# Optimization experiments

Measured on AMD Instinct MI355X. Metric: run time of the kernel, lower is better.

The kernel has to match this reference:

```python
import jax, jax.numpy as jnp
import numpy as np

B, NF, FD, ND, C, K, L = 32, 64, 64, 256, 8, 6, 2  # batch, num_frames(feat), fused_dim, nodes, edge channels, neighbors, layers


def setup_inputs() -> dict:
    key = jax.random.key(0)
    ks = jax.random.split(key, 6)
    s = lambda k, shape: jax.random.normal(k, shape, jnp.float32) * 0.05
    return {
        "fused": jax.random.normal(ks[0], (B, NF, FD), jnp.float32),
        "w1": s(ks[1], (NF, FD, FD)),
        "b1": jnp.zeros((NF, 1, FD), jnp.float32),
        "w2": s(ks[2], (NF, FD, ND)),
        "b2": jnp.zeros((NF, 1, ND), jnp.float32),
        "edge_qk_w": s(ks[3], (2 * C * NF, NF)),
        "ga_qk_w": s(ks[4], (L, 2 * NF, NF)),
        "ga_qk_b": jnp.zeros((L, 2 * NF), jnp.float32),
        "ga_w": jnp.ones((L, 1, C), jnp.float32),
    }


def _spec_norm(w):
    # per-node spectral normalization (torch does this in-place under no_grad)
    n = jax.lax.stop_gradient(jnp.linalg.norm(w, ord=2, axis=(1, 2), keepdims=True))
    return w / jnp.clip(n, 1e-6, None)


def _forward(fused, w1, b1, w2, b2, edge_qk_w, ga_qk_w, ga_qk_b, ga_w):
    scale = NF ** -0.5
    # --- MultiNodeMlp (per-frame node-wise MLP) ---
    h = jnp.einsum('bni,nij->bnj', fused, _spec_norm(w1)) + b1[:, 0]
    h = jax.nn.gelu(h, approximate=False)
    conv = jnp.einsum('bni,nio->bno', h, _spec_norm(w2)) + b2[:, 0]  # [B,NF,ND]
    x = conv.transpose(0, 2, 1)  # node features [B,ND,NF]

    # --- EdgeLayer: multi-channel attention + top-k clip + double normalization ---
    qk = (x @ edge_qk_w.T).reshape(B, ND, 2, C, NF)
    q = qk[:, :, 0].transpose(0, 2, 1, 3)  # [B,C,ND,NF]
    k = qk[:, :, 1].transpose(0, 2, 1, 3)
    attn = jax.nn.softmax(jnp.einsum('bcnf,bcmf->bcnm', q, k) * scale, axis=-1)
    sum_edge = jax.lax.stop_gradient(attn).sum(axis=1)            # [B,ND,ND]
    top_idx = jax.lax.top_k(sum_edge, K)[1]                       # [B,ND,K]
    onehot = jnp.clip(jax.nn.one_hot(top_idx, ND, dtype=attn.dtype).sum(axis=2), 0.0, 1.0)
    mask = jnp.maximum(onehot, jnp.eye(ND, dtype=attn.dtype))[:, None]  # [B,1,ND,ND]
    masked = mask * attn
    nr = masked / (masked.sum(-1, keepdims=True) + 1e-6)
    nc = nr / (nr.sum(-2, keepdims=True) + 1e-6)
    edge = jnp.einsum('bcnd,bcmd->bcnm', nr, nc)                  # norm_row @ norm_col^T

    # --- LipschitzGraph: residual invertible graph attention layers ---
    eye = jnp.eye(NF, dtype=x.dtype)
    for l in range(L):
        W, bqk, wch = ga_qk_w[l], ga_qk_b[l], ga_w[l]
        xs = jax.nn.sigmoid(jax.nn.elu(x))
        qkx = xs @ W.T + bqk                                       # [B,ND,2NF]
        qg, kg = qkx[..., :NF], qkx[..., NF:]
        a = jax.nn.softmax(jnp.einsum('bnf,bmf->bnm', qg, kg) * scale, axis=-1)
        ne = a[:, None] * edge                                     # [B,C,ND,ND]
        ne = ne / (ne.sum(-1, keepdims=True) + 1e-6)
        ne = jnp.einsum('bcnd,c->bnd', ne, (wch / wch.sum())[0])
        dot = W[:NF] @ W[NF:].T * scale
        lip = jax.lax.stop_gradient(jnp.linalg.norm(eye + 2.0 * dot, ord=2)) + 5.0
        x = x + (ne @ xs) / lip
    return x


def reference(fused, w1, b1, w2, b2, edge_qk_w, ga_qk_w, ga_qk_b, ga_w):
    return _forward(fused, w1, b1, w2, b2, edge_qk_w, ga_qk_w, ga_qk_b, ga_w)
```

## Files before the change

kernel.cpp:

```cpp
#include <hip/hip_runtime.h>
#include <float.h>
#include <math.h>


typedef short bf8t __attribute__((ext_vector_type(8)));
typedef float f4t __attribute__((ext_vector_type(4)));

static __device__ __forceinline__ unsigned short f2bf(float x) {
  union { float f; unsigned u; } v; v.f = x;
  unsigned r = (v.u + 0x7FFFu + ((v.u >> 16) & 1u)) >> 16;
  return (unsigned short)r;
}
static __device__ __forceinline__ float bf2f(unsigned short s) {
  union { unsigned u; float f; } v; v.u = ((unsigned)s) << 16; return v.f;
}
static __device__ __forceinline__ float bf2f_lo(unsigned u) {
  union { unsigned u; float f; } v; v.u = u << 16; return v.f;
}
static __device__ __forceinline__ float bf2f_hi(unsigned u) {
  union { unsigned u; float f; } v; v.u = u & 0xFFFF0000u; return v.f;
}
static __device__ __forceinline__ float dot3_pair(unsigned uqh, unsigned uql,
                                                  unsigned ukh, unsigned ukl) {
  float s = bf2f_lo(uqh) * (bf2f_lo(ukh) + bf2f_lo(ukl)) + bf2f_lo(uql) * bf2f_lo(ukh);
  s += bf2f_hi(uqh) * (bf2f_hi(ukh) + bf2f_hi(ukl)) + bf2f_hi(uql) * bf2f_hi(ukh);
  return s;
}
static __device__ __forceinline__ void split8(const float* __restrict__ p,
                                              bf8t* hi, bf8t* lo) {
  float4 v0 = *(const float4*)(p);
  float4 v1 = *(const float4*)(p + 4);
  float v[8] = {v0.x, v0.y, v0.z, v0.w, v1.x, v1.y, v1.z, v1.w};
#pragma unroll
  for (int j = 0; j < 8; j++) {
    unsigned short h = f2bf(v[j]);
    (*hi)[j] = (short)h;
    (*lo)[j] = (short)f2bf(v[j] - bf2f(h));
  }
}

#define SPAD 68

static __device__ __forceinline__ void mm_mfma(
    const float* __restrict__ A, const float* __restrict__ B,
    float* __restrict__ C, int t, float scale, int addI, int transposeStore) {
  int wv = t >> 6, l = t & 63;
  int m16 = l & 15, quad = l >> 4;
  bf8t ah[2], al[2];
  const float* ap = A + (size_t)(16 * wv + m16) * SPAD + quad * 8;
  split8(ap, &ah[0], &al[0]);
  split8(ap + 32, &ah[1], &al[1]);
  f4t acc[4];
#pragma unroll
  for (int ct = 0; ct < 4; ct++) {
    bf8t bh[2], bl[2];
    const float* bp = B + (size_t)(ct * 16 + m16) * SPAD + quad * 8;
    split8(bp, &bh[0], &bl[0]);
    split8(bp + 32, &bh[1], &bl[1]);
    f4t a = (f4t){0.f, 0.f, 0.f, 0.f};
    a = __builtin_amdgcn_mfma_f32_16x16x32_bf16(al[0], bh[0], a, 0, 0, 0);
    a = __builtin_amdgcn_mfma_f32_16x16x32_bf16(ah[0], bl[0], a, 0, 0, 0);
    a = __builtin_amdgcn_mfma_f32_16x16x32_bf16(ah[0], bh[0], a, 0, 0, 0);
    a = __builtin_amdgcn_mfma_f32_16x16x32_bf16(al[1], bh[1], a, 0, 0, 0);
    a = __builtin_amdgcn_mfma_f32_16x16x32_bf16(ah[1], bl[1], a, 0, 0, 0);
    a = __builtin_amdgcn_mfma_f32_16x16x32_bf16(ah[1], bh[1], a, 0, 0, 0);
    acc[ct] = a;
  }
#pragma unroll
  for (int ct = 0; ct < 4; ct++)
#pragma unroll
    for (int j = 0; j < 4; j++) {
      int i0 = 16 * wv + quad * 4 + j;
      int j0 = ct * 16 + m16;
      float v = acc[ct][j] * scale + ((addI && i0 == j0) ? 1.0f : 0.0f);
      if (transposeStore) C[(size_t)j0 * SPAD + i0] = v;
      else C[(size_t)i0 * SPAD + j0] = v;
    }
}

static __device__ __forceinline__ void mm_sq_norm(
    const float* __restrict__ A, float* __restrict__ C, int t,
    float* __restrict__ redm) {
  int wv = t >> 6, l = t & 63;
  int m16 = l & 15, quad = l >> 4;
  bf8t ah[2], al[2];
  const float* ap = A + (size_t)(16 * wv + m16) * SPAD + quad * 8;
  split8(ap, &ah[0], &al[0]);
  split8(ap + 32, &ah[1], &al[1]);
  f4t acc[4];
#pragma unroll
  for (int ct = 0; ct < 4; ct++) {
    bf8t bh[2], bl[2];
    const float* bp = A + (size_t)(ct * 16 + m16) * SPAD + quad * 8;
    split8(bp, &bh[0], &bl[0]);
    split8(bp + 32, &bh[1], &bl[1]);
    f4t a = (f4t){0.f, 0.f, 0.f, 0.f};
    a = __builtin_amdgcn_mfma_f32_16x16x32_bf16(al[0], bh[0], a, 0, 0, 0);
    a = __builtin_amdgcn_mfma_f32_16x16x32_bf16(ah[0], bl[0], a, 0, 0, 0);
    a = __builtin_amdgcn_mfma_f32_16x16x32_bf16(ah[0], bh[0], a, 0, 0, 0);
    a = __builtin_amdgcn_mfma_f32_16x16x32_bf16(al[1], bh[1], a, 0, 0, 0);
    a = __builtin_amdgcn_mfma_f32_16x16x32_bf16(ah[1], bl[1], a, 0, 0, 0);
    a = __builtin_amdgcn_mfma_f32_16x16x32_bf16(ah[1], bh[1], a, 0, 0, 0);
    acc[ct] = a;
  }
  float mx = 0.f;
#pragma unroll
  for (int ct = 0; ct < 4; ct++)
#pragma unroll
    for (int j = 0; j < 4; j++) mx = fmaxf(mx, fabsf(acc[ct][j]));
#pragma unroll
  for (int m = 1; m < 64; m <<= 1) mx = fmaxf(mx, __shfl_xor(mx, m, 64));
  if (l == 0) redm[wv] = mx;
  __syncthreads();
  float gmx = fmaxf(fmaxf(redm[0], redm[1]), fmaxf(redm[2], redm[3]));
  float sc = 1.0f / fmaxf(gmx, 1e-30f);
#pragma unroll
  for (int ct = 0; ct < 4; ct++)
#pragma unroll
    for (int j = 0; j < 4; j++)
      C[(size_t)(16 * wv + quad * 4 + j) * SPAD + ct * 16 + m16] = acc[ct][j] * sc;
}

static __device__ __forceinline__ void gram_mfma(
    const float* __restrict__ Ag, int ncols, float* __restrict__ S,
    float* __restrict__ G, int t) {
  int wv = t >> 6, l = t & 63;
  int m16 = l & 15, quad = l >> 4;
  f4t acc[4];
#pragma unroll
  for (int ct = 0; ct < 4; ct++) acc[ct] = (f4t){0.f, 0.f, 0.f, 0.f};
  for (int cc = 0; cc < ncols; cc += 64) {
    if (cc) __syncthreads();
    for (int i = t; i < 1024; i += 256) {
      int r = i >> 4, qq = i & 15;
      float4 v = *(const float4*)(Ag + (size_t)r * ncols + cc + 4 * qq);
      *(float4*)(S + (size_t)r * SPAD + 4 * qq) = v;
    }
    __syncthreads();
    bf8t ah[2], al[2];
    const float* ap = S + (size_t)(16 * wv + m16) * SPAD + quad * 8;
    split8(ap, &ah[0], &al[0]);
    split8(ap + 32, &ah[1], &al[1]);
#pragma unroll
    for (int ct = 0; ct < 4; ct++) {
      bf8t bh[2], bl[2];
      const float* bp = S + (size_t)(ct * 16 + m16) * SPAD + quad * 8;
      split8(bp, &bh[0], &bl[0]);
      split8(bp + 32, &bh[1], &bl[1]);
      f4t a = acc[ct];
      a = __builtin_amdgcn_mfma_f32_16x16x32_bf16(al[0], bh[0], a, 0, 0, 0);
      a = __builtin_amdgcn_mfma_f32_16x16x32_bf16(ah[0], bl[0], a, 0, 0, 0);
      a = __builtin_amdgcn_mfma_f32_16x16x32_bf16(ah[0], bh[0], a, 0, 0, 0);
      a = __builtin_amdgcn_mfma_f32_16x16x32_bf16(al[1], bh[1], a, 0, 0, 0);
      a = __builtin_amdgcn_mfma_f32_16x16x32_bf16(ah[1], bl[1], a, 0, 0, 0);
      a = __builtin_amdgcn_mfma_f32_16x16x32_bf16(ah[1], bh[1], a, 0, 0, 0);
      acc[ct] = a;
    }
  }
  __syncthreads();
#pragma unroll
  for (int ct = 0; ct < 4; ct++)
#pragma unroll
    for (int j = 0; j < 4; j++)
      G[(size_t)(16 * wv + quad * 4 + j) * SPAD + ct * 16 + m16] = acc[ct][j];
}

static __device__ __forceinline__ float power_rayleigh(
    const float* __restrict__ G4m, const float* __restrict__ Gm, int iters, int i) {
  float row[64];
#pragma unroll
  for (int j = 0; j < 16; j++)
    *(float4*)(row + 4 * j) = *(const float4*)(G4m + (size_t)i * SPAD + 4 * j);
  float v = 1.0f + 0.3f * sinf(7.0f * (float)(i + 1));
  for (int it = 0; it < iters; it++) {
    float u0 = 0.f, u1 = 0.f, u2 = 0.f, u3 = 0.f;
#pragma unroll
    for (int j = 0; j < 16; j++) {
      u0 += row[4 * j + 0] * __shfl(v, 4 * j + 0, 64);
      u1 += row[4 * j + 1] * __shfl(v, 4 * j + 1, 64);
      u2 += row[4 * j + 2] * __shfl(v, 4 * j + 2, 64);
      u3 += row[4 * j + 3] * __shfl(v, 4 * j + 3, 64);
    }
    float u = (u0 + u1) + (u2 + u3);
    float ss = u * u;
#pragma unroll
    for (int m = 1; m < 64; m <<= 1) ss += __shfl_xor(ss, m, 64);
    v = u * rsqrtf(fmaxf(ss, 1e-30f));
  }
  float rowg[64];
#pragma unroll
  for (int j = 0; j < 16; j++)
    *(float4*)(rowg + 4 * j) = *(const float4*)(Gm + (size_t)i * SPAD + 4 * j);
  float u0 = 0.f, u1 = 0.f, u2 = 0.f, u3 = 0.f;
#pragma unroll
  for (int j = 0; j < 16; j++) {
    u0 += rowg[4 * j + 0] * __shfl(v, 4 * j + 0, 64);
    u1 += rowg[4 * j + 1] * __shfl(v, 4 * j + 1, 64);
    u2 += rowg[4 * j + 2] * __shfl(v, 4 * j + 2, 64);
    u3 += rowg[4 * j + 3] * __shfl(v, 4 * j + 3, 64);
  }
  float u = (u0 + u1) + (u2 + u3);
  float d = v * u;
#pragma unroll
  for (int m = 1; m < 64; m <<= 1) d += __shfl_xor(d, m, 64);
  return d;
}

__global__ __launch_bounds__(256) void speclip_kernel(
    const float* __restrict__ w1, const float* __restrict__ w2,
    const float* __restrict__ gaw, float* __restrict__ invsig1,
    float* __restrict__ invsig2, float* __restrict__ lipv) {
  __shared__ float Sa[64 * SPAD];
  __shared__ float Sb[64 * SPAD];
  __shared__ float G[64 * SPAD];
  __shared__ float redm[4];
  int t = threadIdx.x;
  int blk = blockIdx.x;
  if (blk < 128) {
    int n = blk & 63;
    const float* A = (blk < 64) ? (w1 + (size_t)n * 4096) : (w2 + (size_t)n * 16384);
    int ncols = (blk < 64) ? 64 : 256;
    gram_mfma(A, ncols, Sa, G, t);
    __syncthreads();
    mm_mfma(G, G, Sa, t, 1.f, 0, 0);
    __syncthreads();
    mm_sq_norm(Sa, Sb, t, redm);  __syncthreads();
    mm_sq_norm(Sb, Sa, t, redm);  __syncthreads();
    mm_sq_norm(Sa, Sb, t, redm);  __syncthreads();
    mm_sq_norm(Sb, Sa, t, redm);  __syncthreads();
    mm_sq_norm(Sa, Sb, t, redm);  __syncthreads();
    mm_sq_norm(Sb, Sa, t, redm);  __syncthreads();
    if (t < 64) {
      float d = power_rayleigh(Sa, G, 2, t);
      if (t == 0) {
        float sg = sqrtf(fmaxf(d, 0.f));
        float inv = 1.0f / fmaxf(sg, 1e-6f);
        if (blk < 64) invsig1[n] = inv; else invsig2[n] = inv;
      }
    }
  } else {
    int l = blk - 128;
    const float* Wb = gaw + (size_t)l * 8192;
    for (int i = t; i < 1024; i += 256) {
      int r = i >> 4, qq = i & 15;
      *(float4*)(Sa + (size_t)r * SPAD + 4 * qq) = *(const float4*)(Wb + r * 64 + 4 * qq);
      *(float4*)(Sb + (size_t)r * SPAD + 4 * qq) = *(const float4*)(Wb + 4096 + r * 64 + 4 * qq);
    }
    __syncthreads();
    mm_mfma(Sa, Sb, G, t, 0.25f, 1, 1);
    __syncthreads();
    mm_mfma(G, G, Sa, t, 1.f, 0, 0);
    __syncthreads();
    mm_sq_norm(Sa, Sb, t, redm);  __syncthreads();
    mm_sq_norm(Sb, G, t, redm);   __syncthreads();
    mm_sq_norm(G, Sb, t, redm);   __syncthreads();
    mm_sq_norm(Sb, G, t, redm);   __syncthreads();
    mm_sq_norm(G, Sb, t, redm);   __syncthreads();
    mm_sq_norm(Sb, G, t, redm);   __syncthreads();
    if (t < 64) {
      float d = power_rayleigh(G, Sa, 2, t);
      if (t == 0) lipv[l] = sqrtf(fmaxf(d, 0.f)) + 5.0f;
    }
  }
}

__global__ __launch_bounds__(256) void h_kernel(
    const float* __restrict__ fused, const float* __restrict__ w1,
    const float* __restrict__ b1, const float* __restrict__ invsig1,
    float* __restrict__ h) {
  __shared__ float fr[256];
  int t = threadIdx.x;
  int blk = blockIdx.x;
  int ng = blk & 15;
  fr[t] = fused[(size_t)blk * 256 + t];
  __syncthreads();
  int nl = t >> 6, j = t & 63;
  int n = ng * 4 + nl;
  float is1 = invsig1[n];
  const float* fp = fr + nl * 64;
  const float* wp = w1 + (size_t)n * 4096 + j;
  float acc = 0.f;
  for (int i = 0; i < 64; i++) acc += fp[i] * wp[i * 64];
  acc = acc * is1 + b1[n * 64 + j];
  float g = 0.5f * acc * (1.0f + erff(acc * 0.70710678118654752440f));
  h[(size_t)blk * 256 + t] = g;
}

__global__ __launch_bounds__(256) void conv_kernel(
    const float* __restrict__ h, const float* __restrict__ w2,
    const float* __restrict__ b2, const float* __restrict__ invsig2,
    float* __restrict__ x) {
  __shared__ float hr[4][64];
  int t = threadIdx.x;
  int blk = blockIdx.x;
  int b = blk >> 4, ng = blk & 15;
  int n0 = ng * 4;
  {
    int r = t >> 6, i = t & 63;
    hr[r][i] = h[((size_t)b * 64 + n0 + r) * 64 + i];
  }
  __syncthreads();
  const float* w0p = w2 + ((size_t)(n0 + 0) * 64) * 256 + t;
  const float* w1p = w2 + ((size_t)(n0 + 1) * 64) * 256 + t;
  const float* w2p = w2 + ((size_t)(n0 + 2) * 64) * 256 + t;
  const float* w3p = w2 + ((size_t)(n0 + 3) * 64) * 256 + t;
  float a0 = 0.f, a1 = 0.f, a2 = 0.f, a3 = 0.f;
  for (int i = 0; i < 64; i++) {
    a0 += hr[0][i] * w0p[(size_t)i * 256];
    a1 += hr[1][i] * w1p[(size_t)i * 256];
    a2 += hr[2][i] * w2p[(size_t)i * 256];
    a3 += hr[3][i] * w3p[(size_t)i * 256];
  }
  float4 o;
  o.x = a0 * invsig2[n0 + 0] + b2[(n0 + 0) * 256 + t];
  o.y = a1 * invsig2[n0 + 1] + b2[(n0 + 1) * 256 + t];
  o.z = a2 * invsig2[n0 + 2] + b2[(n0 + 2) * 256 + t];
  o.w = a3 * invsig2[n0 + 3] + b2[(n0 + 3) * 256 + t];
  *(float4*)(x + ((size_t)b * 256 + t) * 64 + n0) = o;
}

__global__ __launch_bounds__(256, 2) void qk_kernel(
    const float* __restrict__ x, const float* __restrict__ eqk,
    unsigned short* __restrict__ qhi, unsigned short* __restrict__ qlo,
    unsigned short* __restrict__ khi, unsigned short* __restrict__ klo) {
  int t = threadIdx.x;
  int blk = blockIdx.x;
  int xcd = blk & 7;
  int y = blk >> 3;
  int rh = y & 1;
  int c = (y >> 1) & 7;
  int b = (y >> 4) * 8 + xcd;
  int wv = t >> 6, l = t & 63;
  int m16 = l & 15, quad = l >> 4;
  int row0 = rh * 128 + wv * 32;

  bf8t ah[2][2], al[2][2];
#pragma unroll
  for (int rt = 0; rt < 2; rt++) {
    const float* xp = x + ((size_t)b * 256 + row0 + rt * 16 + m16) * 64 + quad * 8;
    split8(xp, &ah[rt][0], &al[rt][0]);
    split8(xp + 32, &ah[rt][1], &al[rt][1]);
  }
#pragma unroll
  for (int mat = 0; mat < 2; mat++) {
    const float* Wbase = eqk + ((size_t)(mat * 8 + c) * 64) * 64;
    unsigned short* ohi = mat ? khi : qhi;
    unsigned short* olo = mat ? klo : qlo;
#pragma unroll
    for (int ct = 0; ct < 4; ct++) {
      bf8t bh[2], bl[2];
      const float* wp = Wbase + (size_t)(ct * 16 + m16) * 64 + quad * 8;
      split8(wp, &bh[0], &bl[0]);
      split8(wp + 32, &bh[1], &bl[1]);
#pragma unroll
      for (int rt = 0; rt < 2; rt++) {
        f4t a = (f4t){0.f, 0.f, 0.f, 0.f};
        a = __builtin_amdgcn_mfma_f32_16x16x32_bf16(al[rt][0], bh[0], a, 0, 0, 0);
        a = __builtin_amdgcn_mfma_f32_16x16x32_bf16(ah[rt][0], bl[0], a, 0, 0, 0);
        a = __builtin_amdgcn_mfma_f32_16x16x32_bf16(ah[rt][0], bh[0], a, 0, 0, 0);
        a = __builtin_amdgcn_mfma_f32_16x16x32_bf16(al[rt][1], bh[1], a, 0, 0, 0);
        a = __builtin_amdgcn_mfma_f32_16x16x32_bf16(ah[rt][1], bl[1], a, 0, 0, 0);
        a = __builtin_amdgcn_mfma_f32_16x16x32_bf16(ah[rt][1], bh[1], a, 0, 0, 0);
#pragma unroll
        for (int j = 0; j < 4; j++) {
          int n = row0 + rt * 16 + quad * 4 + j;
          int f = ct * 16 + m16;
          size_t o = (((size_t)b * 8 + c) * 256 + n) * 64 + f;
          float v = a[j];
          unsigned short hh = f2bf(v);
          ohi[o] = hh;
          olo[o] = f2bf(v - bf2f(hh));
        }
      }
    }
  }
}

__global__ __launch_bounds__(256, 2) void transpose_kernel(
    const float* __restrict__ in, float* __restrict__ out) {
  __shared__ float T[256 * 65];
  int t = threadIdx.x;
  size_t base = (size_t)blockIdx.x * 16384;
  const float4* in4 = (const float4*)(in + base);
  float4* out4 = (float4*)(out + base);
  for (int i = t; i < 4096; i += 256) {
    int n = i >> 4, fq = i & 15;
    float4 v = in4[i];
    float* dst = T + n * 65 + 4 * fq;
    dst[0] = v.x; dst[1] = v.y; dst[2] = v.z; dst[3] = v.w;
  }
  __syncthreads();
  for (int i = t; i < 4096; i += 256) {
    int f = i >> 6, m4 = i & 63;
    float4 o;
    o.x = T[(4 * m4 + 0) * 65 + f];
    o.y = T[(4 * m4 + 1) * 65 + f];
    o.z = T[(4 * m4 + 2) * 65 + f];
    o.w = T[(4 * m4 + 3) * 65 + f];
    out4[f * 64 + m4] = o;
  }
}

__global__ __launch_bounds__(256, 2) void attn_kernel(
    const unsigned short* __restrict__ qhi, const unsigned short* __restrict__ qlo,
    const unsigned short* __restrict__ khi, const unsigned short* __restrict__ klo,
    float* __restrict__ seP, float* __restrict__ mxb, float* __restrict__ rzb) {
  int t = threadIdx.x;
  int blk = blockIdx.x;
  int xcd = blk & 7;
  int y = blk >> 3;
  int b = xcd * 4 + (y & 3);
  int cg = (y >> 2) & 3;
  int ng = y >> 4;
  int wv = t >> 6, l = t & 63;
  int m16 = l & 15, quad = l >> 4;
  int n0w = ng * 64 + wv * 16;

  f4t sum_acc[16];
#pragma unroll
  for (int mt = 0; mt < 16; mt++) sum_acc[mt] = (f4t){0.f, 0.f, 0.f, 0.f};

  for (int ci = 0; ci < 2; ci++) {
    int c = cg * 2 + ci;
    size_t sl = ((size_t)b * 8 + c) * 16384;
    const bf8t* qh = (const bf8t*)(qhi + sl + (size_t)(n0w + m16) * 64 + quad * 8);
    const bf8t* ql = (const bf8t*)(qlo + sl + (size_t)(n0w + m16) * 64 + quad * 8);
    bf8t ah0 = qh[0], ah1 = qh[4];
    bf8t al0 = ql[0], al1 = ql[4];
    f4t acc[16];
#pragma unroll
    for (int mt = 0; mt < 16; mt++) acc[mt] = (f4t){0.f, 0.f, 0.f, 0.f};
    for (int mt = 0; mt < 16; mt++) {
      const bf8t* kh = (const bf8t*)(khi + sl + (size_t)(mt * 16 + m16) * 64 + quad * 8);
      const bf8t* kl = (const bf8t*)(klo + sl + (size_t)(mt * 16 + m16) * 64 + quad * 8);
      bf8t bh0 = kh[0], bh1 = kh[4];
      bf8t bl0 = kl[0], bl1 = kl[4];
      f4t a = acc[mt];
      a = __builtin_amdgcn_mfma_f32_16x16x32_bf16(al0, bh0, a, 0, 0, 0);
      a = __builtin_amdgcn_mfma_f32_16x16x32_bf16(ah0, bl0, a, 0, 0, 0);
      a = __builtin_amdgcn_mfma_f32_16x16x32_bf16(ah0, bh0, a, 0, 0, 0);
      a = __builtin_amdgcn_mfma_f32_16x16x32_bf16(al1, bh1, a, 0, 0, 0);
      a = __builtin_amdgcn_mfma_f32_16x16x32_bf16(ah1, bl1, a, 0, 0, 0);
      a = __builtin_amdgcn_mfma_f32_16x16x32_bf16(ah1, bh1, a, 0, 0, 0);
      acc[mt] = a;
    }
#pragma unroll
    for (int j = 0; j < 4; j++) {
      float mx = -FLT_MAX;
#pragma unroll
      for (int mt = 0; mt < 16; mt++) mx = fmaxf(mx, acc[mt][j]);
      mx = fmaxf(mx, __shfl_xor(mx, 1, 64));
      mx = fmaxf(mx, __shfl_xor(mx, 2, 64));
      mx = fmaxf(mx, __shfl_xor(mx, 4, 64));
      mx = fmaxf(mx, __shfl_xor(mx, 8, 64));
      float mxl = mx * 0.125f;
      float e[16];
      float z = 0.f;
#pragma unroll
      for (int mt = 0; mt < 16; mt++) {
        e[mt] = expf(acc[mt][j] * 0.125f - mxl);
        z += e[mt];
      }
      z += __shfl_xor(z, 1, 64);
      z += __shfl_xor(z, 2, 64);
      z += __shfl_xor(z, 4, 64);
      z += __shfl_xor(z, 8, 64);
      int n = n0w + quad * 4 + j;
      if (m16 == 0) {
        mxb[((size_t)b * 8 + c) * 256 + n] = mxl;
        rzb[((size_t)b * 8 + c) * 256 + n] = z;
      }
      float zi = 1.0f / z;
#pragma unroll
      for (int mt = 0; mt < 16; mt++) sum_acc[mt][j] += e[mt] * zi;
    }
  }
#pragma unroll
  for (int mt = 0; mt < 16; mt++) {
#pragma unroll
    for (int j = 0; j < 4; j++) {
      int n = n0w + quad * 4 + j;
      seP[((size_t)(cg * 32 + b) * 256 + n) * 256 + mt * 16 + m16] = sum_acc[mt][j];
    }
  }
}

__global__ __launch_bounds__(256) void topsel_kernel(
    const float* __restrict__ seP, int* __restrict__ idx7) {
  __shared__ float seL[64 * 260];
  __shared__ float cv[64][24];
  __shared__ int cidx[64][24];
  int t = threadIdx.x;
  int b = blockIdx.x >> 2, rg = blockIdx.x & 3;
  int n0 = rg * 64;
  const float* s0 = seP + ((size_t)b * 256 + n0) * 256;
  const float* s1 = seP + ((size_t)(32 + b) * 256 + n0) * 256;
  const float* s2 = seP + ((size_t)(64 + b) * 256 + n0) * 256;
  const float* s3 = seP + ((size_t)(96 + b) * 256 + n0) * 256;
  for (int i = t; i < 4096; i += 256) {
    int m4 = i & 63, r = i >> 6;
    float4 v0 = ((const float4*)(s0 + (size_t)r * 256))[m4];
    float4 v1 = ((const float4*)(s1 + (size_t)r * 256))[m4];
    float4 v2 = ((const float4*)(s2 + (size_t)r * 256))[m4];
    float4 v3 = ((const float4*)(s3 + (size_t)r * 256))[m4];
    float4 s;
    s.x = (v0.x + v1.x) + (v2.x + v3.x);
    s.y = (v0.y + v1.y) + (v2.y + v3.y);
    s.z = (v0.z + v1.z) + (v2.z + v3.z);
    s.w = (v0.w + v1.w) + (v2.w + v3.w);
    *(float4*)(seL + r * 260 + m4 * 4) = s;
  }
  __syncthreads();
  {
    int r = t >> 2, qtr = t & 3;
    float tv[6]; int ti[6];
#pragma unroll
    for (int s = 0; s < 6; s++) { tv[s] = -FLT_MAX; ti[s] = 1 << 30; }
    for (int i = 0; i < 64; i++) {
      int m = 4 * i + qtr;
      float val = seL[r * 260 + m];
      if (val > tv[5]) {
        tv[5] = val; ti[5] = m;
#pragma unroll
        for (int s = 5; s > 0; s--) {
          if (tv[s] > tv[s - 1]) {
            float tmv = tv[s]; tv[s] = tv[s - 1]; tv[s - 1] = tmv;
            int tmi = ti[s]; ti[s] = ti[s - 1]; ti[s - 1] = tmi;
          }
        }
      }
    }
#pragma unroll
    for (int s = 0; s < 6; s++) { cv[r][qtr * 6 + s] = tv[s]; cidx[r][qtr * 6 + s] = ti[s]; }
  }
  __syncthreads();
  if (t < 64) {
    int r = t, n = n0 + r;
    int sel[7];
    for (int round = 0; round < 6; round++) {
      float best = -FLT_MAX; int bi = 1 << 30, bs = 0;
      for (int j = 0; j < 24; j++) {
        float v = cv[r][j]; int id = cidx[r][j];
        if (v > best || (v == best && id < bi)) { best = v; bi = id; bs = j; }
      }
      sel[round] = bi;
      cv[r][bs] = -FLT_MAX;
    }
    bool dup = false;
#pragma unroll
    for (int j = 0; j < 6; j++) dup = dup || (sel[j] == n);
    sel[6] = dup ? -1 : n;
#pragma unroll
    for (int j = 0; j < 7; j++) idx7[((size_t)b * 256 + n) * 7 + j] = sel[j];
  }
}

__global__ __launch_bounds__(256) void nr_kernel(
    const unsigned short* __restrict__ qhi, const unsigned short* __restrict__ qlo,
    const unsigned short* __restrict__ khi, const unsigned short* __restrict__ klo,
    const float* __restrict__ mxb, const float* __restrict__ rzb,
    const int* __restrict__ idx7, float* __restrict__ nrv,
    float* __restrict__ colsum) {
  __shared__ int idxs[7];
  __shared__ float attL[56];
  int t = threadIdx.x;
  int b = blockIdx.x >> 8, n = blockIdx.x & 255;
  if (t < 7) idxs[t] = idx7[(size_t)blockIdx.x * 7 + t];
  __syncthreads();
  int task = t >> 2, l4 = t & 3;
  if (task < 56) {
    int c = task / 7, j = task - c * 7;
    int d = idxs[j];
    float s = 0.f;
    if (d >= 0) {
      size_t qo = (((size_t)b * 8 + c) * 256 + n) * 64 + l4 * 16;
      size_t ko = (((size_t)b * 8 + c) * 256 + d) * 64 + l4 * 16;
      const uint4* qh4 = (const uint4*)(qhi + qo);
      const uint4* ql4 = (const uint4*)(qlo + qo);
      const uint4* kh4 = (const uint4*)(khi + ko);
      const uint4* kl4 = (const uint4*)(klo + ko);
#pragma unroll
      for (int g = 0; g < 2; g++) {
        uint4 uqh = qh4[g], uql = ql4[g], ukh = kh4[g], ukl = kl4[g];
        s += dot3_pair(uqh.x, uql.x, ukh.x, ukl.x);
        s += dot3_pair(uqh.y, uql.y, ukh.y, ukl.y);
        s += dot3_pair(uqh.z, uql.z, ukh.z, ukl.z);
        s += dot3_pair(uqh.w, uql.w, ukh.w, ukl.w);
      }
    }
    s += __shfl_xor(s, 1, 64);
    s += __shfl_xor(s, 2, 64);
    if (l4 == 0) {
      float att = 0.f;
      if (d >= 0) {
        float logit = s * 0.125f;
        att = expf(logit - mxb[((size_t)b * 8 + c) * 256 + n]) / rzb[((size_t)b * 8 + c) * 256 + n];
      }
      attL[task] = att;
    }
  }
  __syncthreads();
  if (t < 8) {
    float rs = 0.f;
#pragma unroll
    for (int j = 0; j < 7; j++) rs += attL[t * 7 + j];
    float ri = 1.0f / (rs + 1e-6f);
#pragma unroll
    for (int j = 0; j < 7; j++) {
      float nv = attL[t * 7 + j] * ri;
      nrv[(((size_t)b * 8 + t) * 256 + n) * 7 + j] = nv;
      int d = idxs[j];
      if (d >= 0) atomicAdd(&colsum[((size_t)b * 8 + t) * 256 + d], nv);
    }
  }
}

__global__ __launch_bounds__(256, 3) void edge_kernel(
    const int* __restrict__ idx7, const float* __restrict__ nrv,
    const float* __restrict__ colsum, unsigned short* __restrict__ edge) {
  __shared__ unsigned short ncT[256 * 64];
  __shared__ short idxL[256 * 8];
  __shared__ float nrvL[256 * 8];
  int t = threadIdx.x;
  int blk = blockIdx.x;
  int b = blk >> 5, c = (blk >> 2) & 7, mq = blk & 3;
  int m0 = mq * 64;
  for (int i = t; i < 8192; i += 256) ((unsigned int*)ncT)[i] = 0u;
  for (int i = t; i < 2048; i += 256) {
    int r = i >> 3, j = i & 7;
    if (j < 7) {
      idxL[i] = (short)idx7[(size_t)b * 1792 + r * 7 + j];
      nrvL[i] = nrv[((size_t)b * 8 + c) * 1792 + r * 7 + j];
    } else {
      idxL[i] = -1;
      nrvL[i] = 0.f;
    }
  }
  __syncthreads();
  for (int i = t; i < 448; i += 256) {
    int mi = i / 7, j = i - mi * 7;
    int m = m0 + mi;
    int d = idxL[m * 8 + j];
    if (d >= 0) {
      float cs = colsum[((size_t)b * 8 + c) * 256 + d];
      ncT[d * 64 + mi] = f2bf(nrvL[m * 8 + j] / (cs + 1e-6f));
    }
  }
  __syncthreads();
  int wv = t >> 6, l = t & 63;
  int half = l >> 5, p = l & 31;
  const unsigned int* ncP = (const unsigned int*)ncT;
  unsigned int* eb = (unsigned int*)(edge + (((size_t)b * 8 + c) * 256) * 256);
  for (int nn = 0; nn < 32; nn++) {
    int n = nn * 8 + wv * 2 + half;
    int4 iv = *(const int4*)(idxL + n * 8);
    float4 w0 = *(const float4*)(nrvL + n * 8);
    float4 w1 = *(const float4*)(nrvL + n * 8 + 4);
    float a0 = 0.f, a1 = 0.f;
    int d;
    unsigned int pr;
    d = (int)(short)(iv.x & 0xFFFF);
    if (d >= 0) { pr = ncP[d * 32 + p]; a0 += w0.x * bf2f_lo(pr); a1 += w0.x * bf2f_hi(pr); }
    d = iv.x >> 16;
    if (d >= 0) { pr = ncP[d * 32 + p]; a0 += w0.y * bf2f_lo(pr); a1 += w0.y * bf2f_hi(pr); }
    d = (int)(short)(iv.y & 0xFFFF);
    if (d >= 0) { pr = ncP[d * 32 + p]; a0 += w0.z * bf2f_lo(pr); a1 += w0.z * bf2f_hi(pr); }
    d = iv.y >> 16;
    if (d >= 0) { pr = ncP[d * 32 + p]; a0 += w0.w * bf2f_lo(pr); a1 += w0.w * bf2f_hi(pr); }
    d = (int)(short)(iv.z & 0xFFFF);
    if (d >= 0) { pr = ncP[d * 32 + p]; a0 += w1.x * bf2f_lo(pr); a1 += w1.x * bf2f_hi(pr); }
    d = iv.z >> 16;
    if (d >= 0) { pr = ncP[d * 32 + p]; a0 += w1.y * bf2f_lo(pr); a1 += w1.y * bf2f_hi(pr); }
    d = (int)(short)(iv.w & 0xFFFF);
    if (d >= 0) { pr = ncP[d * 32 + p]; a0 += w1.z * bf2f_lo(pr); a1 += w1.z * bf2f_hi(pr); }
    unsigned int packo = (unsigned int)f2bf(a0) | ((unsigned int)f2bf(a1) << 16);
    eb[n * 128 + (m0 >> 1) + p] = packo;
  }
}

static __device__ __forceinline__ float selu1(float v) {
  float e = (v > 0.f) ? v : expm1f(v);
  return 1.0f / (1.0f + expf(-e));
}
__global__ __launch_bounds__(256, 1) void qkx_kernel(
    const float* __restrict__ x, const float* __restrict__ gaw,
    const float* __restrict__ gab, int l, float* __restrict__ xs,
    float* __restrict__ qg, float* __restrict__ kg) {
  __shared__ float xsL[64 * 64];
  int t = threadIdx.x;
  int b = blockIdx.x >> 2, nt = blockIdx.x & 3;
  int f = t & 63, part = t >> 6;
  float wq[64], wk[64];
  const float4* Wq4 = (const float4*)(gaw + (size_t)l * 8192 + f * 64);
  const float4* Wk4 = (const float4*)(gaw + (size_t)l * 8192 + (64 + f) * 64);
#pragma unroll
  for (int j = 0; j < 16; j++) {
    float4 aa = Wq4[j];
    wq[4 * j + 0] = aa.x; wq[4 * j + 1] = aa.y; wq[4 * j + 2] = aa.z; wq[4 * j + 3] = aa.w;
    float4 bb = Wk4[j];
    wk[4 * j + 0] = bb.x; wk[4 * j + 1] = bb.y; wk[4 * j + 2] = bb.z; wk[4 * j + 3] = bb.w;
  }
  float bq = gab[l * 128 + f], bk = gab[l * 128 + 64 + f];
  for (int i = t; i < 1024; i += 256) {
    float4 v = ((const float4*)(x + ((size_t)b * 256 + nt * 64) * 64))[i];
    float4 o;
    o.x = selu1(v.x); o.y = selu1(v.y); o.z = selu1(v.z); o.w = selu1(v.w);
    ((float4*)xsL)[i] = o;
    ((float4*)(xs + ((size_t)b * 256 + nt * 64) * 64))[i] = o;
  }
  __syncthreads();
  for (int i = 0; i < 16; i++) {
    int nl = part * 16 + i;
    const float4* xr = (const float4*)(xsL + nl * 64);
    float aq = 0.f, ak = 0.f;
#pragma unroll
    for (int j = 0; j < 16; j++) {
      float4 v = xr[j];
      aq += v.x * wq[4 * j] + v.y * wq[4 * j + 1] + v.z * wq[4 * j + 2] + v.w * wq[4 * j + 3];
      ak += v.x * wk[4 * j] + v.y * wk[4 * j + 1] + v.z * wk[4 * j + 2] + v.w * wk[4 * j + 3];
    }
    int n = nt * 64 + nl;
    qg[((size_t)b * 256 + n) * 64 + f] = aq + bq;
    kg[((size_t)b * 256 + n) * 64 + f] = ak + bk;
  }
}

__global__ __launch_bounds__(256, 2) void ga_attn_kernel(
    const float* __restrict__ qg, const float* __restrict__ kgT,
    float* __restrict__ a) {
  int t = threadIdx.x;
  int b = blockIdx.x >> 3, nt = blockIdx.x & 7;
  int n0 = nt * 32;
  int wv = t >> 6, l = t & 63;
  const float* kb = kgT + (size_t)b * 16384 + 4 * l;
  const float* qb = qg + ((size_t)b * 256 + n0 + wv * 8) * 64;
  float acc[8][4];
#pragma unroll
  for (int r = 0; r < 8; r++)
#pragma unroll
    for (int j = 0; j < 4; j++) acc[r][j] = 0.f;
#pragma unroll 4
  for (int kq4 = 0; kq4 < 64; kq4 += 4) {
    float4 kv0 = *(const float4*)(kb + (kq4 + 0) * 256);
    float4 kv1 = *(const float4*)(kb + (kq4 + 1) * 256);
    float4 kv2 = *(const float4*)(kb + (kq4 + 2) * 256);
    float4 kv3 = *(const float4*)(kb + (kq4 + 3) * 256);
#pragma unroll
    for (int r = 0; r < 8; r++) {
      float4 qv = *(const float4*)(qb + r * 64 + kq4);
      acc[r][0] += qv.x * kv0.x + qv.y * kv1.x + qv.z * kv2.x + qv.w * kv3.x;
      acc[r][1] += qv.x * kv0.y + qv.y * kv1.y + qv.z * kv2.y + qv.w * kv3.y;
      acc[r][2] += qv.x * kv0.z + qv.y * kv1.z + qv.z * kv2.z + qv.w * kv3.z;
      acc[r][3] += qv.x * kv0.w + qv.y * kv1.w + qv.z * kv2.w + qv.w * kv3.w;
    }
  }
#pragma unroll
  for (int r = 0; r < 8; r++) {
    float l0 = acc[r][0] * 0.125f, l1 = acc[r][1] * 0.125f;
    float l2 = acc[r][2] * 0.125f, l3 = acc[r][3] * 0.125f;
    float mx = fmaxf(fmaxf(l0, l1), fmaxf(l2, l3));
#pragma unroll
    for (int m = 1; m < 64; m <<= 1) mx = fmaxf(mx, __shfl_xor(mx, m, 64));
    float e0 = expf(l0 - mx), e1 = expf(l1 - mx), e2 = expf(l2 - mx), e3 = expf(l3 - mx);
    float z = e0 + e1 + e2 + e3;
#pragma unroll
    for (int m = 1; m < 64; m <<= 1) z += __shfl_xor(z, m, 64);
    float zi = 1.0f / z;
    int n = n0 + wv * 8 + r;
    float4 o;
    o.x = e0 * zi; o.y = e1 * zi; o.z = e2 * zi; o.w = e3 * zi;
    ((float4*)(a + ((size_t)b * 256 + n) * 256))[l] = o;
  }
}

__global__ __launch_bounds__(256) void upd_kernel(
    const float* __restrict__ a, const unsigned short* __restrict__ edge,
    const float* __restrict__ xs, const float* __restrict__ gaww,
    const float* __restrict__ lipv, int l, float* __restrict__ x) {
  __shared__ float tt[4][8][260];
  __shared__ float ne3[4][256];
  __shared__ float parts[4][4][64];
  __shared__ float dred[32][8];
  __shared__ float dinv[4][8];
  __shared__ float wcL[8];
  __shared__ float lipi;
  int t = threadIdx.x;
  int b = blockIdx.x >> 6, nq = blockIdx.x & 63;
  int n0 = nq * 4;
  if (t == 0) {
    float s = 0.f;
    float wtmp[8];
    for (int c = 0; c < 8; c++) { wtmp[c] = gaww[l * 8 + c]; s += wtmp[c]; }
    for (int c = 0; c < 8; c++) wcL[c] = wtmp[c] / s;
    lipi = 1.0f / lipv[l];
  }
#pragma unroll
  for (int r = 0; r < 4; r++) {
    float av = a[((size_t)b * 256 + n0 + r) * 256 + t];
#pragma unroll
    for (int c = 0; c < 8; c++)
      tt[r][c][t] = av * bf2f(edge[(((size_t)b * 8 + c) * 256 + n0 + r) * 256 + t]);
  }
  __syncthreads();
  {
    int rc = t >> 3, i = t & 7;
    int r = rc >> 3, c = rc & 7;
    float p = 0.f;
#pragma unroll
    for (int kq = 0; kq < 32; kq++) p += tt[r][c][i + 8 * kq];
    dred[rc][i] = p;
  }
  __syncthreads();
  if (t < 32) {
    float s = 0.f;
#pragma unroll
    for (int i = 0; i < 8; i++) s += dred[t][i];
    dinv[t >> 3][t & 7] = 1.0f / (s + 1e-6f);
  }
  __syncthreads();
#pragma unroll
  for (int r = 0; r < 4; r++) {
    float s = 0.f;
#pragma unroll
    for (int c = 0; c < 8; c++) s += wcL[c] * tt[r][c][t] * dinv[r][c];
    ne3[r][t] = s;
  }
  __syncthreads();
  {
    int f = t & 63, part = t >> 6;
    float a0 = 0.f, a1 = 0.f, a2 = 0.f, a3 = 0.f;
    for (int mm = 0; mm < 64; mm++) {
      int m = part * 64 + mm;
      float xv = xs[((size_t)b * 256 + m) * 64 + f];
      a0 += ne3[0][m] * xv;
      a1 += ne3[1][m] * xv;
      a2 += ne3[2][m] * xv;
      a3 += ne3[3][m] * xv;
    }
    parts[0][part][f] = a0;
    parts[1][part][f] = a1;
    parts[2][part][f] = a2;
    parts[3][part][f] = a3;
  }
  __syncthreads();
  {
    int r = t >> 6, f = t & 63;
    float dx = parts[r][0][f] + parts[r][1][f] + parts[r][2][f] + parts[r][3][f];
    x[((size_t)b * 256 + n0 + r) * 64 + f] += dx * lipi;
  }
}

extern "C" void kernel_launch(void* const* d_in, const int* in_sizes, int n_in,
                              void* d_out, int out_size, void* d_ws, size_t ws_size,
                              hipStream_t stream) {
  (void)in_sizes; (void)n_in; (void)out_size; (void)ws_size;
  const float* fused = (const float*)d_in[0];
  const float* w1 = (const float*)d_in[1];
  const float* b1 = (const float*)d_in[2];
  const float* w2 = (const float*)d_in[3];
  const float* b2 = (const float*)d_in[4];
  const float* eqk = (const float*)d_in[5];
  const float* gaw = (const float*)d_in[6];
  const float* gab = (const float*)d_in[7];
  const float* gaww = (const float*)d_in[8];
  float* x = (float*)d_out;
  char* ws = (char*)d_ws;
  size_t off = 0;
  auto alloc = [&](size_t bytes) -> char* {
    char* p = ws + off;
    off += (bytes + 1023) & ~(size_t)1023;
    return p;
  };
  float* invsig1 = (float*)alloc(64 * 4);
  float* invsig2 = (float*)alloc(64 * 4);
  float* lipv = (float*)alloc(2 * 4);
  float* h = (float*)alloc((size_t)32 * 64 * 64 * 4);
  unsigned short* qhi = (unsigned short*)alloc((size_t)32 * 8 * 256 * 64 * 2);
  unsigned short* qlo = (unsigned short*)alloc((size_t)32 * 8 * 256 * 64 * 2);
  unsigned short* khi = (unsigned short*)alloc((size_t)32 * 8 * 256 * 64 * 2);
  unsigned short* klo = (unsigned short*)alloc((size_t)32 * 8 * 256 * 64 * 2);
  char* sep_edge = alloc((size_t)4 * 32 * 256 * 256 * 4);
  float* seP = (float*)sep_edge;
  unsigned short* edge = (unsigned short*)sep_edge;
  float* mxb = (float*)alloc((size_t)65536 * 4);
  float* rzb = (float*)alloc((size_t)65536 * 4);
  int* idx7 = (int*)alloc((size_t)8192 * 7 * 4);
  float* nrv = (float*)alloc((size_t)65536 * 7 * 4);
  float* colsum = (float*)alloc((size_t)65536 * 4);
  float* xs = (float*)alloc((size_t)524288 * 4);
  float* qg = (float*)alloc((size_t)524288 * 4);
  float* kg = (float*)alloc((size_t)524288 * 4);
  float* a = (float*)alloc((size_t)32 * 256 * 256 * 4);
  float* kgT = (float*)alloc((size_t)524288 * 4);

  speclip_kernel<<<130, 256, 0, stream>>>(w1, w2, gaw, invsig1, invsig2, lipv);
  h_kernel<<<512, 256, 0, stream>>>(fused, w1, b1, invsig1, h);
  conv_kernel<<<512, 256, 0, stream>>>(h, w2, b2, invsig2, x);
  qk_kernel<<<512, 256, 0, stream>>>(x, eqk, qhi, qlo, khi, klo);
  attn_kernel<<<512, 256, 0, stream>>>(qhi, qlo, khi, klo, seP, mxb, rzb);
  hipMemsetAsync(colsum, 0, (size_t)65536 * 4, stream);
  topsel_kernel<<<128, 256, 0, stream>>>(seP, idx7);
  nr_kernel<<<8192, 256, 0, stream>>>(qhi, qlo, khi, klo, mxb, rzb, idx7, nrv, colsum);
  edge_kernel<<<1024, 256, 0, stream>>>(idx7, nrv, colsum, edge);
  for (int l = 0; l < 2; l++) {
    qkx_kernel<<<128, 256, 0, stream>>>(x, gaw, gab, l, xs, qg, kg);
    transpose_kernel<<<32, 256, 0, stream>>>(kg, kgT);
    ga_attn_kernel<<<256, 256, 0, stream>>>(qg, kgT, a);
    upd_kernel<<<2048, 256, 0, stream>>>(a, edge, xs, gaww, lipv, l, x);
  }
}
```

Before: 394.8 us.

## Split attention channels across waves and reduce softmax sums via shared memory

The attention kernel now runs 512 threads per block, with each half of the waves handling one of the two channels in parallel instead of looping over channels sequentially. Per-channel softmax probabilities are summed in a padded shared-memory tile in two halves. Results are then written to global memory as coalesced float4 rows instead of scattered scalar stores. This aims at more parallelism per block and better store coalescing, at the cost of extra LDS traffic, barriers and higher register pressure from the stricter launch bounds.

After: 393.5 us. About the same (-0.3%).

```diff
diff --git a/kernel.cpp b/kernel.cpp
--- a/kernel.cpp
+++ b/kernel.cpp
@@ -401,10 +401,11 @@
   }
 }
 
-__global__ __launch_bounds__(256, 2) void attn_kernel(
+__global__ __launch_bounds__(512, 4) void attn_kernel(
     const unsigned short* __restrict__ qhi, const unsigned short* __restrict__ qlo,
     const unsigned short* __restrict__ khi, const unsigned short* __restrict__ klo,
     float* __restrict__ seP, float* __restrict__ mxb, float* __restrict__ rzb) {
+  __shared__ float sE[32 * 260];
   int t = threadIdx.x;
   int blk = blockIdx.x;
   int xcd = blk & 7;
@@ -412,76 +413,91 @@
   int b = xcd * 4 + (y & 3);
   int cg = (y >> 2) & 3;
   int ng = y >> 4;
-  int wv = t >> 6, l = t & 63;
+  int wave = t >> 6;
+  int ci = wave >> 2;
+  int wv = wave & 3;
+  int l = t & 63;
   int m16 = l & 15, quad = l >> 4;
   int n0w = ng * 64 + wv * 16;
-
-  f4t sum_acc[16];
-#pragma unroll
-  for (int mt = 0; mt < 16; mt++) sum_acc[mt] = (f4t){0.f, 0.f, 0.f, 0.f};
-
-  for (int ci = 0; ci < 2; ci++) {
-    int c = cg * 2 + ci;
-    size_t sl = ((size_t)b * 8 + c) * 16384;
-    const bf8t* qh = (const bf8t*)(qhi + sl + (size_t)(n0w + m16) * 64 + quad * 8);
-    const bf8t* ql = (const bf8t*)(qlo + sl + (size_t)(n0w + m16) * 64 + quad * 8);
-    bf8t ah0 = qh[0], ah1 = qh[4];
-    bf8t al0 = ql[0], al1 = ql[4];
-    f4t acc[16];
-#pragma unroll
-    for (int mt = 0; mt < 16; mt++) acc[mt] = (f4t){0.f, 0.f, 0.f, 0.f};
+  int c = cg * 2 + ci;
+
+  size_t sl = ((size_t)b * 8 + c) * 16384;
+  const bf8t* qh = (const bf8t*)(qhi + sl + (size_t)(n0w + m16) * 64 + quad * 8);
+  const bf8t* ql = (const bf8t*)(qlo + sl + (size_t)(n0w + m16) * 64 + quad * 8);
+  bf8t ah0 = qh[0], ah1 = qh[4];
+  bf8t al0 = ql[0], al1 = ql[4];
+  f4t acc[16];
+#pragma unroll
+  for (int mt = 0; mt < 16; mt++) acc[mt] = (f4t){0.f, 0.f, 0.f, 0.f};
+  for (int mt = 0; mt < 16; mt++) {
+    const bf8t* kh = (const bf8t*)(khi + sl + (size_t)(mt * 16 + m16) * 64 + quad * 8);
+    const bf8t* kl = (const bf8t*)(klo + sl + (size_t)(mt * 16 + m16) * 64 + quad * 8);
+    bf8t bh0 = kh[0], bh1 = kh[4];
+    bf8t bl0 = kl[0], bl1 = kl[4];
+    f4t a = acc[mt];
+    a = __builtin_amdgcn_mfma_f32_16x16x32_bf16(al0, bh0, a, 0, 0, 0);
+    a = __builtin_amdgcn_mfma_f32_16x16x32_bf16(ah0, bl0, a, 0, 0, 0);
+    a = __builtin_amdgcn_mfma_f32_16x16x32_bf16(ah0, bh0, a, 0, 0, 0);
+    a = __builtin_amdgcn_mfma_f32_16x16x32_bf16(al1, bh1, a, 0, 0, 0);
+    a = __builtin_amdgcn_mfma_f32_16x16x32_bf16(ah1, bl1, a, 0, 0, 0);
+    a = __builtin_amdgcn_mfma_f32_16x16x32_bf16(ah1, bh1, a, 0, 0, 0);
+    acc[mt] = a;
+  }
+#pragma unroll
+  for (int j = 0; j < 4; j++) {
+    float mx = -FLT_MAX;
+#pragma unroll
+    for (int mt = 0; mt < 16; mt++) mx = fmaxf(mx, acc[mt][j]);
+    mx = fmaxf(mx, __shfl_xor(mx, 1, 64));
+    mx = fmaxf(mx, __shfl_xor(mx, 2, 64));
+    mx = fmaxf(mx, __shfl_xor(mx, 4, 64));
+    mx = fmaxf(mx, __shfl_xor(mx, 8, 64));
+    float mxl = mx * 0.125f;
+    float z = 0.f;
+#pragma unroll
     for (int mt = 0; mt < 16; mt++) {
-      const bf8t* kh = (const bf8t*)(khi + sl + (size_t)(mt * 16 + m16) * 64 + quad * 8);
-      const bf8t* kl = (const bf8t*)(klo + sl + (size_t)(mt * 16 + m16) * 64 + quad * 8);
-      bf8t bh0 = kh[0], bh1 = kh[4];
-      bf8t bl0 = kl[0], bl1 = kl[4];
-      f4t a = acc[mt];
-      a = __builtin_amdgcn_mfma_f32_16x16x32_bf16(al0, bh0, a, 0, 0, 0);
-      a = __builtin_amdgcn_mfma_f32_16x16x32_bf16(ah0, bl0, a, 0, 0, 0);
-      a = __builtin_amdgcn_mfma_f32_16x16x32_bf16(ah0, bh0, a, 0, 0, 0);
-      a = __builtin_amdgcn_mfma_f32_16x16x32_bf16(al1, bh1, a, 0, 0, 0);
-      a = __builtin_amdgcn_mfma_f32_16x16x32_bf16(ah1, bl1, a, 0, 0, 0);
-      a = __builtin_amdgcn_mfma_f32_16x16x32_bf16(ah1, bh1, a, 0, 0, 0);
-      acc[mt] = a;
-    }
-#pragma unroll
-    for (int j = 0; j < 4; j++) {
-      float mx = -FLT_MAX;
-#pragma unroll
-      for (int mt = 0; mt < 16; mt++) mx = fmaxf(mx, acc[mt][j]);
-      mx = fmaxf(mx, __shfl_xor(mx, 1, 64));
-      mx = fmaxf(mx, __shfl_xor(mx, 2, 64));
-      mx = fmaxf(mx, __shfl_xor(mx, 4, 64));
-      mx = fmaxf(mx, __shfl_xor(mx, 8, 64));
-      float mxl = mx * 0.125f;
-      float e[16];
-      float z = 0.f;
-#pragma unroll
-      for (int mt = 0; mt < 16; mt++) {
-        e[mt] = expf(acc[mt][j] * 0.125f - mxl);
-        z += e[mt];
-      }
-      z += __shfl_xor(z, 1, 64);
-      z += __shfl_xor(z, 2, 64);
-      z += __shfl_xor(z, 4, 64);
-      z += __shfl_xor(z, 8, 64);
-      int n = n0w + quad * 4 + j;
-      if (m16 == 0) {
-        mxb[((size_t)b * 8 + c) * 256 + n] = mxl;
-        rzb[((size_t)b * 8 + c) * 256 + n] = z;
-      }
-      float zi = 1.0f / z;
-#pragma unroll
-      for (int mt = 0; mt < 16; mt++) sum_acc[mt][j] += e[mt] * zi;
-    }
-  }
-#pragma unroll
-  for (int mt = 0; mt < 16; mt++) {
-#pragma unroll
-    for (int j = 0; j < 4; j++) {
-      int n = n0w + quad * 4 + j;
-      seP[((size_t)(cg * 32 + b) * 256 + n) * 256 + mt * 16 + m16] = sum_acc[mt][j];
-    }
+      float e = expf(acc[mt][j] * 0.125f - mxl);
+      acc[mt][j] = e;
+      z += e;
+    }
+    z += __shfl_xor(z, 1, 64);
+    z += __shfl_xor(z, 2, 64);
+    z += __shfl_xor(z, 4, 64);
+    z += __shfl_xor(z, 8, 64);
+    int n = n0w + quad * 4 + j;
+    if (m16 == 0) {
+      mxb[((size_t)b * 8 + c) * 256 + n] = mxl;
+      rzb[((size_t)b * 8 + c) * 256 + n] = z;
+    }
+    float zi = 1.0f / z;
+#pragma unroll
+    for (int mt = 0; mt < 16; mt++) acc[mt][j] *= zi;
+  }
+  for (int half = 0; half < 2; half++) {
+    if (ci == 0 && (wv >> 1) == half) {
+      int r0 = (wv & 1) * 16;
+#pragma unroll
+      for (int mt = 0; mt < 16; mt++)
+#pragma unroll
+        for (int j = 0; j < 4; j++)
+          sE[(r0 + quad * 4 + j) * 260 + mt * 16 + m16] = acc[mt][j];
+    }
+    __syncthreads();
+    if (ci == 1 && (wv >> 1) == half) {
+      int r0 = (wv & 1) * 16;
+#pragma unroll
+      for (int mt = 0; mt < 16; mt++)
+#pragma unroll
+        for (int j = 0; j < 4; j++)
+          sE[(r0 + quad * 4 + j) * 260 + mt * 16 + m16] += acc[mt][j];
+    }
+    __syncthreads();
+    float4* dst4 = (float4*)(seP + (((size_t)cg * 32 + b) * 256 + ng * 64 + half * 32) * 256);
+    for (int i = t; i < 2048; i += 512) {
+      int r = i >> 6, c4 = i & 63;
+      dst4[i] = *(const float4*)(sE + r * 260 + c4 * 4);
+    }
+    if (half == 0) __syncthreads();
   }
 }
 
@@ -897,7 +913,7 @@
   h_kernel<<<512, 256, 0, stream>>>(fused, w1, b1, invsig1, h);
   conv_kernel<<<512, 256, 0, stream>>>(h, w2, b2, invsig2, x);
   qk_kernel<<<512, 256, 0, stream>>>(x, eqk, qhi, qlo, khi, klo);
-  attn_kernel<<<512, 256, 0, stream>>>(qhi, qlo, khi, klo, seP, mxb, rzb);
+  attn_kernel<<<512, 512, 0, stream>>>(qhi, qlo, khi, klo, seP, mxb, rzb);
   hipMemsetAsync(colsum, 0, (size_t)65536 * 4, stream);
   topsel_kernel<<<128, 256, 0, stream>>>(seP, idx7);
   nr_kernel<<<8192, 256, 0, stream>>>(qhi, qlo, khi, klo, mxb, rzb, idx7, nrv, colsum);
```
